# Kernel optimization log

Measured on AMD Instinct MI355X. Metric: run time of the kernel, lower is better.

## Reference

```python
import jax, jax.numpy as jnp
import numpy as np

N, E, G = 20000, 320000, 64
F_NODE, F_EDGE = 16, 16
NHID, M, NLAYER, NOUT = 128, 4, 3, 64
EPS = 1e-5


def setup_inputs() -> dict:
    key = jax.random.key(0)
    ks = jax.random.split(key, 20)
    w = lambda k, s: (jax.random.normal(k, s, jnp.float32) * 0.1)
    inp = {
        "x_node": jax.random.normal(ks[0], (N, F_NODE), jnp.float32),
        "edge_attr": jax.random.normal(ks[1], (E, F_EDGE), jnp.float32),
        "edge_index": jax.random.randint(ks[2], (2, E), 0, N, dtype=jnp.int32),
        "batch": jnp.sort(jax.random.randint(ks[3], (N,), 0, G, dtype=jnp.int32)),
        "additional_x": jax.random.normal(ks[4], (N, 1, M), jnp.float32),
        # input encoder MLP(F_NODE->NHID, 1 layer): Linear + BN + ReLU
        "W_in": w(ks[5], (NHID, F_NODE)), "b_in": jnp.zeros((NHID,)),
        "g_in": jnp.ones((NHID,)), "bt_in": jnp.zeros((NHID,)),
        # Linear2: weight (NHID, NHID+1), bias (NHID,)
        "W_l2": w(ks[6], (NHID, NHID + 1)), "b_l2": jnp.zeros((NHID,)),
        # per-layer edge encoders MLP(F_EDGE->NHID, 1 layer)
        "W_edge": w(ks[7], (NLAYER, NHID, F_EDGE)), "b_edge": jnp.zeros((NLAYER, NHID)),
        "g_edge": jnp.ones((NLAYER, NHID)), "bt_edge": jnp.zeros((NLAYER, NHID)),
        # per-layer conv linear (bias=False since bn='BN')
        "W_conv": w(ks[8], (NLAYER, NHID, NHID)),
        # per-layer BatchNorm1d(NHID)
        "g_norm": jnp.ones((NLAYER, NHID)), "bt_norm": jnp.zeros((NLAYER, NHID)),
        # output encoder MLP(NHID->NOUT, 2 layers, norm between, no final act)
        "W_out1": w(ks[9], (NOUT, NHID)), "b_out1": jnp.zeros((NOUT,)),
        "g_out": jnp.ones((NOUT,)), "bt_out": jnp.zeros((NOUT,)),
        "W_out2": w(ks[10], (NOUT, NOUT)), "b_out2": jnp.zeros((NOUT,)),
    }
    return inp


def _bn2(x, g, b):  # BatchNorm1d on (R, C), training-mode batch stats
    mu = x.mean(0)
    var = x.var(0)
    return (x - mu) * jax.lax.rsqrt(var + EPS) * g + b


def _bn3(x, g, b):  # BatchNorm1d on (N, C, M): stats over N and M per channel
    mu = x.mean((0, 2), keepdims=True)
    var = x.var((0, 2), keepdims=True)
    return (x - mu) * jax.lax.rsqrt(var + EPS) * g[None, :, None] + b[None, :, None]


def reference(x_node, edge_attr, edge_index, batch, additional_x,
              W_in, b_in, g_in, bt_in, W_l2, b_l2,
              W_edge, b_edge, g_edge, bt_edge, W_conv, g_norm, bt_norm,
              W_out1, b_out1, g_out, bt_out, W_out2, b_out2):
    # --- input encoder: MLP(F_node -> nhid, 1 layer) ---
    h = jax.nn.relu(_bn2(x_node @ W_in.T + b_in, g_in, bt_in))  # (N, NHID)

    # --- Linear2(h, additional_x): faithful to the torch reshapes ---
    n, d = h.shape
    m = additional_x.shape[-1]
    xr = jnp.transpose(additional_x, (2, 1, 0)).reshape(n * m, 1)  # x_r.T.reshape(N*M, -1)
    rand_out = xr @ W_l2[:, -1:].T + b_l2                          # (M*N, NHID)
    main = h @ W_l2[:, :-1] + b_l2                                 # F.linear(x, weight.T[:-1]) == x @ W[:, :-1]
    x = main[:, :, None] + rand_out.reshape(n, -1, m)              # (N, NHID, M)

    src, dst = edge_index[0], edge_index[1]
    prev = x
    for l in range(NLAYER):
        # edge encoder: MLP(F_edge -> nhid, 1 layer)
        e = jax.nn.relu(_bn2(edge_attr @ W_edge[l].T + b_edge[l], g_edge[l], bt_edge[l]))  # (E, NHID)
        # GINE-style conv: sum_j relu(x_j + e_ij), then linear on channel dim (no bias)
        msg = jax.nn.relu(x[src] + e[:, :, None])                  # (E, NHID, M)
        agg = jax.ops.segment_sum(msg, dst, num_segments=n)        # (N, NHID, M)
        h3 = jnp.einsum('ncm,oc->nom', x + agg, W_conv[l])
        h3 = jax.nn.relu(_bn3(h3, g_norm[l], bt_norm[l]))          # norm -> relu (dropout=0)
        x = h3 + prev                                              # residual
        prev = x

    # --- add pooling over graphs ---
    xg = jax.ops.segment_sum(x, batch, num_segments=G)             # (G, NHID, M)
    H1, H2, Mm = xg.shape
    flat = xg.reshape(-1, H2)                                      # faithful to x.view(-1, H2)
    o = jax.nn.relu(_bn2(flat @ W_out1.T + b_out1, g_out, bt_out))
    o = o @ W_out2.T + b_out2                                      # (G*M, NOUT)
    out = o.reshape(H1, o.shape[-1], -1).mean(-1)                  # (G, NOUT)
    return out
```

## Files before the change

kernel.cpp:

```cpp
#include <hip/hip_runtime.h>

constexpr int N_ = 20000, E_ = 320000, G_ = 64;
constexpr int NHID = 128, M_ = 4;
constexpr float EPS = 1e-5f;

#define RFL(v) __builtin_amdgcn_readfirstlane(v)
#define RLF(v, l) __int_as_float(__builtin_amdgcn_readlane(__float_as_int(v), (l)))

__global__ void k_moments(const float* __restrict__ A, int R,
                          float* __restrict__ oSum, float* __restrict__ oOut) {
  __shared__ float ls[64][16];
  int t = threadIdx.x;
  int k = t >> 4, j = t & 15;
  float accO = 0.f, accS = 0.f;
  for (int base = blockIdx.x * 64; base < R; base += gridDim.x * 64) {
    int rows = min(64, R - base);
    for (int i = t; i < rows * 16; i += 256) ls[i >> 4][i & 15] = A[base * 16 + i];
    __syncthreads();
    for (int r = 0; r < rows; ++r) accO += ls[r][k] * ls[r][j];
    if (t < 16) { for (int r = 0; r < rows; ++r) accS += ls[r][t]; }
    __syncthreads();
  }
  atomicAdd(&oOut[t], accO);
  if (t < 16) atomicAdd(&oSum[t], accS);
}

__global__ __launch_bounds__(512) void k_fold(
    const float* __restrict__ momNs, const float* __restrict__ momNo,
    const float* __restrict__ momEs, const float* __restrict__ momEo,
    const float* __restrict__ W_in, const float* __restrict__ b_in,
    const float* __restrict__ g_in, const float* __restrict__ bt_in,
    const float* __restrict__ W_e, const float* __restrict__ b_e,
    const float* __restrict__ g_e, const float* __restrict__ bt_e,
    float* __restrict__ Wf_in, float* __restrict__ bf_in,
    float* __restrict__ Wf_e, float* __restrict__ bf_e) {
  __shared__ float mN[16], oN[256], mE[16], oE[256];
  int t = threadIdx.x;
  if (t < 16) { mN[t] = momNs[t] * (1.f / N_); mE[t] = momEs[t] * (1.f / E_); }
  for (int i = t; i < 256; i += 512) { oN[i] = momNo[i] * (1.f / N_); oE[i] = momEo[i] * (1.f / E_); }
  __syncthreads();
  const float *m, *mo, *wrow; float bb, ggv, btv; float *wout, *boutp;
  if (t < 128) {
    m = mN; mo = oN; wrow = W_in + t * 16; bb = b_in[t]; ggv = g_in[t]; btv = bt_in[t];
    wout = Wf_in + t * 16; boutp = bf_in + t;
  } else {
    int u = t - 128;
    m = mE; mo = oE; wrow = W_e + u * 16; bb = b_e[u]; ggv = g_e[u]; btv = bt_e[u];
    wout = Wf_e + u * 16; boutp = bf_e + u;
  }
  float wl[16];
#pragma unroll
  for (int k = 0; k < 16; ++k) wl[k] = wrow[k];
  float wm = 0.f;
#pragma unroll
  for (int k = 0; k < 16; ++k) wm = fmaf(wl[k], m[k], wm);
  float mu = wm + bb;
  float ey2 = bb * bb + 2.f * bb * wm;
  for (int k = 0; k < 16; ++k) {
#pragma unroll
    for (int j = 0; j < 16; ++j) ey2 = fmaf(wl[k] * wl[j], mo[k * 16 + j], ey2);
  }
  float var = ey2 - mu * mu;
  float s = ggv * rsqrtf(var + EPS);
#pragma unroll
  for (int k = 0; k < 16; ++k) wout[k] = wl[k] * s;
  *boutp = (bb - mu) * s + btv;
}

__global__ __launch_bounds__(128) void k_lin2(
    const float* __restrict__ xn, const float* __restrict__ addx,
    const float* __restrict__ Wf, const float* __restrict__ bf,
    const float* __restrict__ W2, const float* __restrict__ b2,
    float* __restrict__ X) {
  __shared__ float a[4][16];
  __shared__ float h[4][128];
  int c = threadIdx.x;
  int n0 = blockIdx.x * 4;
  if (c < 64) a[c >> 4][c & 15] = xn[n0 * 16 + c];
  __syncthreads();
  float wl[16];
  const float* w = Wf + c * 16;
#pragma unroll
  for (int k = 0; k < 16; ++k) wl[k] = w[k];
  float bfc = bf[c];
#pragma unroll
  for (int nd = 0; nd < 4; ++nd) {
    float acc = bfc;
#pragma unroll
    for (int k = 0; k < 16; ++k) acc = fmaf(a[nd][k], wl[k], acc);
    h[nd][c] = fmaxf(acc, 0.f);
  }
  __syncthreads();
  float b2c = b2[c];
  float mn[4] = {b2c, b2c, b2c, b2c};
#pragma unroll 4
  for (int k = 0; k < 128; ++k) {
    float wv = W2[k * 129 + c];
    mn[0] = fmaf(h[0][k], wv, mn[0]);
    mn[1] = fmaf(h[1][k], wv, mn[1]);
    mn[2] = fmaf(h[2][k], wv, mn[2]);
    mn[3] = fmaf(h[3][k], wv, mn[3]);
  }
  int ccb = (c & 31) * 4;
  float wr0 = W2[(ccb + 0) * 129 + 128], br0 = b2[ccb + 0];
  float wr1 = W2[(ccb + 1) * 129 + 128], br1 = b2[ccb + 1];
  float wr2 = W2[(ccb + 2) * 129 + 128], br2 = b2[ccb + 2];
  float wr3 = W2[(ccb + 3) * 129 + 128], br3 = b2[ccb + 3];
  float4* Xv = reinterpret_cast<float4*>(X);
#pragma unroll
  for (int nd = 0; nd < 4; ++nd) {
    int i = 4 * (n0 + nd) + (c >> 5);
    int id = i / N_;
    int ir = i - id * N_;
    float xr = addx[ir * 4 + id];
    float4 o;
    o.x = mn[nd] + xr * wr0 + br0;
    o.y = mn[nd] + xr * wr1 + br1;
    o.z = mn[nd] + xr * wr2 + br2;
    o.w = mn[nd] + xr * wr3 + br3;
    Xv[(size_t)(n0 + nd) * 128 + c] = o;
  }
}

__global__ void k_hist(const int* __restrict__ ei, int* __restrict__ cnt) {
  int e = blockIdx.x * 256 + threadIdx.x;
  if (e < E_) atomicAdd(&cnt[ei[E_ + e]], 1);
}

__global__ __launch_bounds__(1024) void k_scan(const int* __restrict__ cnt, int* __restrict__ off) {
  __shared__ int wsum[16];
  __shared__ int carrySh;
  int t = threadIdx.x, lane = t & 63, w = t >> 6;
  if (t == 0) carrySh = 0;
  __syncthreads();
  for (int base = 0; base < N_; base += 1024) {
    int v = (base + t < N_) ? cnt[base + t] : 0;
    int s = v;
#pragma unroll
    for (int ofs = 1; ofs < 64; ofs <<= 1) {
      int u = __shfl_up(s, ofs);
      if (lane >= ofs) s += u;
    }
    if (lane == 63) wsum[w] = s;
    int carry = carrySh;
    __syncthreads();
    int pre = 0, tot = 0;
#pragma unroll
    for (int ww = 0; ww < 16; ++ww) {
      int x = wsum[ww];
      pre += (ww < w) ? x : 0;
      tot += x;
    }
    if (base + t < N_) off[base + t] = carry + pre + s - v;
    __syncthreads();
    if (t == 0) carrySh = carry + tot;
    __syncthreads();
  }
  if (t == 0) off[N_] = carrySh;
}

__global__ void k_scatter(const int* __restrict__ ei, const int* __restrict__ off,
                          int* __restrict__ cur, int* __restrict__ csr) {
  int e = blockIdx.x * 256 + threadIdx.x;
  if (e < E_) {
    int d = ei[E_ + e];
    int pidx = atomicAdd(&cur[d], 1);
    csr[off[d] + pidx] = e;
  }
}

__global__ void k_transp(const float* __restrict__ Wc, float* __restrict__ WT4) {
  int i = blockIdx.x * 256 + threadIdx.x;
  if (i >= 3 * 128 * 128) return;
  int l = i >> 14, rest = i & 16383;
  int o = rest >> 7, c = rest & 127;
  WT4[l * 16384 + ((c >> 1) * 64 + (o & 63)) * 4 + (c & 1) * 2 + (o >> 6)] = Wc[i];
}

__global__ void k_init64(int* g) { g[threadIdx.x] = N_; }
__global__ void k_bound(const int* __restrict__ batch, int* __restrict__ gstart) {
  int n = blockIdx.x * 256 + threadIdx.x;
  if (n < N_) atomicMin(&gstart[batch[n]], n);
}
__global__ void k_bound2(const int* __restrict__ gstart, int* __restrict__ gend) {
  int g = threadIdx.x;
  int e = N_;
  for (int gg = g + 1; gg < 64; ++gg) { int s = gstart[gg]; if (s < N_) { e = s; break; } }
  gend[g] = e;
}

__global__ __launch_bounds__(512, 4) void k_aggemm(
    const float* __restrict__ X, const int* __restrict__ ei,
    const float* __restrict__ attr,
    const int* __restrict__ off, const int* __restrict__ csr,
    const float* __restrict__ Wf, const float* __restrict__ bf,
    const float* __restrict__ WT4,
    float* __restrict__ H3, float* __restrict__ bnsum, float* __restrict__ bnsumsq) {
  __shared__ float lW[16384];
  __shared__ float red[512][4];
  int t = threadIdx.x;
  int lane = t & 63;
  int n = blockIdx.x * 8 + (t >> 6);
  {
    const float4* Wg = reinterpret_cast<const float4*>(WT4);
    float4* lW4 = reinterpret_cast<float4*>(lW);
#pragma unroll
    for (int i = 0; i < 8; ++i) lW4[t + i * 512] = Wg[t + i * 512];
  }
  float w0[16], w1[16];
#pragma unroll
  for (int k = 0; k < 16; ++k) { w0[k] = Wf[lane * 16 + k]; w1[k] = Wf[(lane + 64) * 16 + k]; }
  float b0 = bf[lane], b1 = bf[lane + 64];
  const float4* Xv = reinterpret_cast<const float4*>(X);
  const float4* Av = reinterpret_cast<const float4*>(attr);
  float4 acc0 = Xv[(size_t)n * 128 + lane];
  float4 acc1 = Xv[(size_t)n * 128 + 64 + lane];
  __syncthreads();

  int qs = RFL(off[n]);
  int qe = RFL(off[n + 1]);
  if (qs < qe) {
    int last = qe - 1;
#define IDX(Q, EV, SV) { int qq_ = (Q) < last ? (Q) : last; EV = RFL(csr[qq_]); SV = RFL(ei[EV]); }
#define LOADP(SV, EV, X0, X1, AV) \
    X0 = Xv[(size_t)(SV) * 128 + lane]; \
    X1 = Xv[(size_t)(SV) * 128 + 64 + lane]; \
    AV = Av[(size_t)(EV) * 4 + (lane & 3)];
#define ETERM(AVV, CMP, LN, K) { float as_ = RLF(AVV.CMP, LN); \
    ee0 = fmaf(as_, w0[K], ee0); ee1 = fmaf(as_, w1[K], ee1); }
#define EDGE(X0, X1, AV) { \
    float ee0 = b0, ee1 = b1; \
    ETERM(AV, x, 0, 0)  ETERM(AV, y, 0, 1)  ETERM(AV, z, 0, 2)  ETERM(AV, w, 0, 3) \
    ETERM(AV, x, 1, 4)  ETERM(AV, y, 1, 5)  ETERM(AV, z, 1, 6)  ETERM(AV, w, 1, 7) \
    ETERM(AV, x, 2, 8)  ETERM(AV, y, 2, 9)  ETERM(AV, z, 2, 10) ETERM(AV, w, 2, 11) \
    ETERM(AV, x, 3, 12) ETERM(AV, y, 3, 13) ETERM(AV, z, 3, 14) ETERM(AV, w, 3, 15) \
    ee0 = fmaxf(ee0, 0.f); ee1 = fmaxf(ee1, 0.f); \
    acc0.x += fmaxf(X0.x + ee0, 0.f); acc0.y += fmaxf(X0.y + ee0, 0.f); \
    acc0.z += fmaxf(X0.z + ee0, 0.f); acc0.w += fmaxf(X0.w + ee0, 0.f); \
    acc1.x += fmaxf(X1.x + ee1, 0.f); acc1.y += fmaxf(X1.y + ee1, 0.f); \
    acc1.z += fmaxf(X1.z + ee1, 0.f); acc1.w += fmaxf(X1.w + ee1, 0.f); }
    int e0, s0, e1, s1, e2, s2, e3, s3, e4, s4, e5, s5;
    IDX(qs,     e0, s0); IDX(qs + 1, e1, s1); IDX(qs + 2, e2, s2);
    IDX(qs + 3, e3, s3); IDX(qs + 4, e4, s4); IDX(qs + 5, e5, s5);
    float4 x00, x01, av0, x10, x11, av1, x20, x21, av2;
    LOADP(s0, e0, x00, x01, av0);
    LOADP(s1, e1, x10, x11, av1);
    LOADP(s2, e2, x20, x21, av2);
    for (int q = qs; q < qe; q += 3) {
      int n0i, n0s, n1i, n1s, n2i, n2s;
      IDX(q + 6, n0i, n0s); IDX(q + 7, n1i, n1s); IDX(q + 8, n2i, n2s);
      EDGE(x00, x01, av0);
      LOADP(s3, e3, x00, x01, av0);
      if (q + 1 < qe) { EDGE(x10, x11, av1); }
      LOADP(s4, e4, x10, x11, av1);
      if (q + 2 < qe) { EDGE(x20, x21, av2); }
      LOADP(s5, e5, x20, x21, av2);
      e0 = e3; s0 = s3; e1 = e4; s1 = s4; e2 = e5; s2 = s5;
      e3 = n0i; s3 = n0s; e4 = n1i; s4 = n1s; e5 = n2i; s5 = n2s;
    }
#undef EDGE
#undef ETERM
#undef LOADP
#undef IDX
  }
  float4 ha = {0, 0, 0, 0}, hb = {0, 0, 0, 0};
  const float4* Wv = reinterpret_cast<const float4*>(lW);
#pragma unroll 4
  for (int cc = 0; cc < 32; ++cc) {
    float4 wv = Wv[cc * 64 + lane];
    int l0 = 2 * cc, l1 = 2 * cc + 1;
    float za0 = RLF(acc0.x, l0), za1 = RLF(acc0.y, l0), za2 = RLF(acc0.z, l0), za3 = RLF(acc0.w, l0);
    float zb0 = RLF(acc0.x, l1), zb1 = RLF(acc0.y, l1), zb2 = RLF(acc0.z, l1), zb3 = RLF(acc0.w, l1);
    ha.x = fmaf(za0, wv.x, ha.x); ha.y = fmaf(za1, wv.x, ha.y); ha.z = fmaf(za2, wv.x, ha.z); ha.w = fmaf(za3, wv.x, ha.w);
    hb.x = fmaf(za0, wv.y, hb.x); hb.y = fmaf(za1, wv.y, hb.y); hb.z = fmaf(za2, wv.y, hb.z); hb.w = fmaf(za3, wv.y, hb.w);
    ha.x = fmaf(zb0, wv.z, ha.x); ha.y = fmaf(zb1, wv.z, ha.y); ha.z = fmaf(zb2, wv.z, ha.z); ha.w = fmaf(zb3, wv.z, ha.w);
    hb.x = fmaf(zb0, wv.w, hb.x); hb.y = fmaf(zb1, wv.w, hb.y); hb.z = fmaf(zb2, wv.w, hb.z); hb.w = fmaf(zb3, wv.w, hb.w);
  }
#pragma unroll 4
  for (int cc = 32; cc < 64; ++cc) {
    float4 wv = Wv[cc * 64 + lane];
    int l0 = 2 * cc - 64, l1 = 2 * cc - 63;
    float za0 = RLF(acc1.x, l0), za1 = RLF(acc1.y, l0), za2 = RLF(acc1.z, l0), za3 = RLF(acc1.w, l0);
    float zb0 = RLF(acc1.x, l1), zb1 = RLF(acc1.y, l1), zb2 = RLF(acc1.z, l1), zb3 = RLF(acc1.w, l1);
    ha.x = fmaf(za0, wv.x, ha.x); ha.y = fmaf(za1, wv.x, ha.y); ha.z = fmaf(za2, wv.x, ha.z); ha.w = fmaf(za3, wv.x, ha.w);
    hb.x = fmaf(za0, wv.y, hb.x); hb.y = fmaf(za1, wv.y, hb.y); hb.z = fmaf(za2, wv.y, hb.z); hb.w = fmaf(za3, wv.y, hb.w);
    ha.x = fmaf(zb0, wv.z, ha.x); ha.y = fmaf(zb1, wv.z, ha.y); ha.z = fmaf(zb2, wv.z, ha.z); ha.w = fmaf(zb3, wv.z, ha.w);
    hb.x = fmaf(zb0, wv.w, hb.x); hb.y = fmaf(zb1, wv.w, hb.y); hb.z = fmaf(zb2, wv.w, hb.z); hb.w = fmaf(zb3, wv.w, hb.w);
  }
  float4* Hv = reinterpret_cast<float4*>(H3);
  Hv[(size_t)n * 128 + lane] = ha;
  Hv[(size_t)n * 128 + 64 + lane] = hb;
  red[t][0] = ha.x + ha.y + ha.z + ha.w;
  red[t][1] = ha.x * ha.x + ha.y * ha.y + ha.z * ha.z + ha.w * ha.w;
  red[t][2] = hb.x + hb.y + hb.z + hb.w;
  red[t][3] = hb.x * hb.x + hb.y * hb.y + hb.z * hb.z + hb.w * hb.w;
  __syncthreads();
  if (t < 256) {
    int ch = t >> 1, st = t & 1;
    int ln = ch & 63, pr = ch >> 6;
    float v = 0.f;
#pragma unroll
    for (int w8 = 0; w8 < 8; ++w8) v += red[w8 * 64 + ln][pr * 2 + st];
    if (st == 0) atomicAdd(&bnsum[ch], v); else atomicAdd(&bnsumsq[ch], v);
  }
}

__global__ void k_bnres(const float* __restrict__ H3, float* __restrict__ X,
                        const float* __restrict__ bnsum, const float* __restrict__ bnsumsq,
                        const float* __restrict__ gg, const float* __restrict__ bb) {
  constexpr float inv = 1.f / (N_ * 4);
  const float4* Hv = (const float4*)H3;
  float4* Xv = (float4*)X;
  for (int i = blockIdx.x * 256 + threadIdx.x; i < N_ * 128; i += gridDim.x * 256) {
    int o = i & 127;
    float mu = bnsum[o] * inv;
    float var = bnsumsq[o] * inv - mu * mu;
    float sc = gg[o] * rsqrtf(var + EPS);
    float sh = bb[o] - mu * sc;
    float4 h = Hv[i];
    float4 x = Xv[i];
    x.x += fmaxf(fmaf(h.x, sc, sh), 0.f);
    x.y += fmaxf(fmaf(h.y, sc, sh), 0.f);
    x.z += fmaxf(fmaf(h.z, sc, sh), 0.f);
    x.w += fmaxf(fmaf(h.w, sc, sh), 0.f);
    Xv[i] = x;
  }
}

__global__ void k_pool(const float* __restrict__ X, const int* __restrict__ gstart,
                       const int* __restrict__ gend, float* __restrict__ xg) {
  int g = blockIdx.x >> 3, sl = blockIdx.x & 7;
  int t = threadIdx.x;
  int s = gstart[g], e = gend[g];
  float a0 = 0.f, a1 = 0.f;
  for (int n = s + sl; n < e; n += 8) {
    a0 += X[(size_t)n * 512 + t];
    a1 += X[(size_t)n * 512 + t + 256];
  }
  atomicAdd(&xg[g * 512 + t], a0);
  atomicAdd(&xg[g * 512 + t + 256], a1);
}

__global__ void k_head1(const float* __restrict__ xg, const float* __restrict__ W1,
                        const float* __restrict__ b1, float* __restrict__ o1p,
                        float* __restrict__ hsum, float* __restrict__ hsumsq) {
  int t = threadIdx.x;
  int r = blockIdx.x * 4 + (t >> 6), c = t & 63;
  const float* xr = xg + r * 128;
  const float* w = W1 + c * 128;
  float acc = b1[c];
#pragma unroll 8
  for (int k = 0; k < 128; ++k) acc = fmaf(xr[k], w[k], acc);
  o1p[r * 64 + c] = acc;
  atomicAdd(&hsum[c], acc);
  atomicAdd(&hsumsq[c], acc * acc);
}

__global__ void k_head2(const float* __restrict__ o1p, const float* __restrict__ hsum,
                        const float* __restrict__ hsumsq, const float* __restrict__ g_out,
                        const float* __restrict__ bt_out, const float* __restrict__ W2,
                        const float* __restrict__ b2, float* __restrict__ out) {
  __shared__ float s1[4][64];
  __shared__ float s2[4][64];
  int g = blockIdx.x, j = threadIdx.x;
  float mu = hsum[j] * (1.f / 256.f);
  float var = hsumsq[j] * (1.f / 256.f) - mu * mu;
  float sc = g_out[j] * rsqrtf(var + EPS);
  float sh = bt_out[j] - mu * sc;
  for (int r = 0; r < 4; ++r) {
    float v = o1p[(4 * g + r) * 64 + j];
    s1[r][j] = fmaxf(fmaf(v, sc, sh), 0.f);
  }
  __syncthreads();
  for (int r = 0; r < 4; ++r) {
    float acc = b2[j];
#pragma unroll 8
    for (int k = 0; k < 64; ++k) acc = fmaf(s1[r][k], W2[j * 64 + k], acc);
    s2[r][j] = acc;
  }
  __syncthreads();
  float o = 0.f;
#pragma unroll
  for (int k = 0; k < 4; ++k) {
    int t4 = 4 * j + k;
    o += s2[t4 >> 6][t4 & 63];
  }
  out[g * 64 + j] = o * 0.25f;
}

extern "C" void kernel_launch(void* const* d_in, const int* in_sizes, int n_in,
                              void* d_out, int out_size, void* d_ws, size_t ws_size,
                              hipStream_t stream) {
  const float* x_node   = (const float*)d_in[0];
  const float* edge_attr= (const float*)d_in[1];
  const int*   edge_index=(const int*)d_in[2];
  const int*   batch    = (const int*)d_in[3];
  const float* addx     = (const float*)d_in[4];
  const float* W_in  = (const float*)d_in[5];
  const float* b_in  = (const float*)d_in[6];
  const float* g_in  = (const float*)d_in[7];
  const float* bt_in = (const float*)d_in[8];
  const float* W_l2  = (const float*)d_in[9];
  const float* b_l2  = (const float*)d_in[10];
  const float* W_edge  = (const float*)d_in[11];
  const float* b_edge  = (const float*)d_in[12];
  const float* g_edge  = (const float*)d_in[13];
  const float* bt_edge = (const float*)d_in[14];
  const float* W_conv  = (const float*)d_in[15];
  const float* g_norm  = (const float*)d_in[16];
  const float* bt_norm = (const float*)d_in[17];
  const float* W_out1  = (const float*)d_in[18];
  const float* b_out1  = (const float*)d_in[19];
  const float* g_out   = (const float*)d_in[20];
  const float* bt_out  = (const float*)d_in[21];
  const float* W_out2  = (const float*)d_in[22];
  const float* b_out2  = (const float*)d_in[23];
  float* out = (float*)d_out;

  char* base = (char*)d_ws;
  size_t p = 0;
  auto take = [&](size_t bytes) -> char* {
    char* r = base + p;
    p = (p + bytes + 255) & ~(size_t)255;
    return r;
  };
  int*   csr_cnt  = (int*)take((size_t)N_ * 4);
  int*   csr_cur  = (int*)take((size_t)N_ * 4);
  float* momNs    = (float*)take(16 * 4);
  float* momNo    = (float*)take(256 * 4);
  float* momEs    = (float*)take(16 * 4);
  float* momEo    = (float*)take(256 * 4);
  float* bnsum    = (float*)take(3 * 128 * 4);
  float* bnsumsq  = (float*)take(3 * 128 * 4);
  float* xg       = (float*)take(64 * 512 * 4);
  float* hsum     = (float*)take(64 * 4);
  float* hsumsq   = (float*)take(64 * 4);
  size_t zeroEnd = p;
  int*   gstart   = (int*)take(64 * 4);
  int*   gend     = (int*)take(64 * 4);
  int*   csr_off  = (int*)take((size_t)(N_ + 1) * 4);
  int*   csr_edges= (int*)take((size_t)E_ * 4);
  float* Wf_in    = (float*)take(128 * 16 * 4);
  float* bf_in    = (float*)take(128 * 4);
  float* Wf_e     = (float*)take(3 * 128 * 16 * 4);
  float* bf_e     = (float*)take(3 * 128 * 4);
  float* WT4      = (float*)take(3 * 128 * 128 * 4);
  float* o1p      = (float*)take(256 * 64 * 4);
  float* A        = (float*)take((size_t)N_ * 512 * 4);
  float* B        = (float*)take((size_t)N_ * 512 * 4);

  hipMemsetAsync(d_ws, 0, zeroEnd, stream);
  k_init64<<<1, 64, 0, stream>>>(gstart);
  k_moments<<<320, 256, 0, stream>>>(x_node, N_, momNs, momNo);
  k_moments<<<2048, 256, 0, stream>>>(edge_attr, E_, momEs, momEo);
  k_fold<<<1, 512, 0, stream>>>(momNs, momNo, momEs, momEo,
                                W_in, b_in, g_in, bt_in,
                                W_edge, b_edge, g_edge, bt_edge,
                                Wf_in, bf_in, Wf_e, bf_e);
  k_lin2<<<N_ / 4, 128, 0, stream>>>(x_node, addx, Wf_in, bf_in, W_l2, b_l2, A);
  k_hist<<<1250, 256, 0, stream>>>(edge_index, csr_cnt);
  k_scan<<<1, 1024, 0, stream>>>(csr_cnt, csr_off);
  k_scatter<<<1250, 256, 0, stream>>>(edge_index, csr_off, csr_cur, csr_edges);
  k_transp<<<192, 256, 0, stream>>>(W_conv, WT4);
  k_bound<<<79, 256, 0, stream>>>(batch, gstart);
  k_bound2<<<1, 64, 0, stream>>>(gstart, gend);
  for (int l = 0; l < 3; ++l) {
    k_aggemm<<<N_ / 8, 512, 0, stream>>>(A, edge_index, edge_attr, csr_off, csr_edges,
                                         Wf_e + l * 128 * 16, bf_e + l * 128,
                                         WT4 + l * 16384, B,
                                         bnsum + l * 128, bnsumsq + l * 128);
    k_bnres<<<2048, 256, 0, stream>>>(B, A, bnsum + l * 128, bnsumsq + l * 128,
                                      g_norm + l * 128, bt_norm + l * 128);
  }
  k_pool<<<512, 256, 0, stream>>>(A, gstart, gend, xg);
  k_head1<<<64, 256, 0, stream>>>(xg, W_out1, b_out1, o1p, hsum, hsumsq);
  k_head2<<<64, 64, 0, stream>>>(o1p, hsum, hsumsq, g_out, bt_out, W_out2, b_out2, out);
  (void)in_sizes; (void)n_in; (void)out_size; (void)ws_size;
}
```

Measured before the change: 832.4 us.

## Merge prep kernels into fewer launches, enlarge aggemm blocks, hoist BN scale

Fuses the moment, histogram, weight-transpose and graph-boundary kernels into one block-partitioned prep kernel. The scan is merged with the BN fold, and the CSR scatter with the Linear2 kernel, so about eleven launches become three. The graph-boundary computation now uses the sorted batch directly instead of atomicMin plus a second pass. Separately, k_aggemm grows to 1024-thread blocks of 16 nodes so each staged copy of the weight tile in LDS serves more nodes, and k_bnres computes the per-channel BN scale and shift once per block into shared memory. The larger aggemm blocks may lower occupancy or raise register pressure.

```diff
diff --git a/kernel.cpp b/kernel.cpp
--- a/kernel.cpp
+++ b/kernel.cpp
@@ -7,13 +7,12 @@
 #define RFL(v) __builtin_amdgcn_readfirstlane(v)
 #define RLF(v, l) __int_as_float(__builtin_amdgcn_readlane(__float_as_int(v), (l)))
 
-__global__ void k_moments(const float* __restrict__ A, int R,
-                          float* __restrict__ oSum, float* __restrict__ oOut) {
-  __shared__ float ls[64][16];
-  int t = threadIdx.x;
+__device__ __forceinline__ void moments_body(
+    const float* __restrict__ A, int R, float* __restrict__ oSum, float* __restrict__ oOut,
+    int bid, int nb, int t, float ls[64][16]) {
   int k = t >> 4, j = t & 15;
   float accO = 0.f, accS = 0.f;
-  for (int base = blockIdx.x * 64; base < R; base += gridDim.x * 64) {
+  for (int base = bid * 64; base < R; base += nb * 64) {
     int rows = min(64, R - base);
     for (int i = t; i < rows * 16; i += 256) ls[i >> 4][i & 15] = A[base * 16 + i];
     __syncthreads();
@@ -25,7 +24,41 @@
   if (t < 16) atomicAdd(&oSum[t], accS);
 }
 
-__global__ __launch_bounds__(512) void k_fold(
+__global__ __launch_bounds__(256) void k_prep(
+    const float* __restrict__ xn, const float* __restrict__ attr,
+    const int* __restrict__ ei, const int* __restrict__ batch,
+    const float* __restrict__ Wc,
+    float* __restrict__ momNs, float* __restrict__ momNo,
+    float* __restrict__ momEs, float* __restrict__ momEo,
+    int* __restrict__ cnt, float* __restrict__ WT4, int* __restrict__ gs) {
+  __shared__ float ls[64][16];
+  int b = blockIdx.x, t = threadIdx.x;
+  if (b < 320) {
+    moments_body(xn, N_, momNs, momNo, b, 320, t, ls);
+  } else if (b < 2368) {
+    moments_body(attr, E_, momEs, momEo, b - 320, 2048, t, ls);
+  } else if (b < 3618) {
+    int e = (b - 2368) * 256 + t;
+    if (e < E_) atomicAdd(&cnt[ei[E_ + e]], 1);
+  } else if (b < 3810) {
+    int i = (b - 3618) * 256 + t;
+    if (i < 3 * 128 * 128) {
+      int l = i >> 14, rest = i & 16383;
+      int o = rest >> 7, c = rest & 127;
+      WT4[l * 16384 + ((c >> 1) * 64 + (o & 63)) * 4 + (c & 1) * 2 + (o >> 6)] = Wc[i];
+    }
+  } else {
+    int n = (b - 3810) * 256 + t;
+    if (n < N_) {
+      int bn = batch[n];
+      int bp = (n == 0) ? -1 : batch[n - 1];
+      for (int g = bp + 1; g <= bn; ++g) gs[g] = n;
+      if (n == N_ - 1) { for (int g = bn + 1; g <= 64; ++g) gs[g] = N_; }
+    }
+  }
+}
+
+__global__ __launch_bounds__(1024) void k_fold_scan(
     const float* __restrict__ momNs, const float* __restrict__ momNo,
     const float* __restrict__ momEs, const float* __restrict__ momEo,
     const float* __restrict__ W_in, const float* __restrict__ b_in,
@@ -33,50 +66,97 @@
     const float* __restrict__ W_e, const float* __restrict__ b_e,
     const float* __restrict__ g_e, const float* __restrict__ bt_e,
     float* __restrict__ Wf_in, float* __restrict__ bf_in,
-    float* __restrict__ Wf_e, float* __restrict__ bf_e) {
-  __shared__ float mN[16], oN[256], mE[16], oE[256];
+    float* __restrict__ Wf_e, float* __restrict__ bf_e,
+    const int* __restrict__ cnt, int* __restrict__ off) {
   int t = threadIdx.x;
-  if (t < 16) { mN[t] = momNs[t] * (1.f / N_); mE[t] = momEs[t] * (1.f / E_); }
-  for (int i = t; i < 256; i += 512) { oN[i] = momNo[i] * (1.f / N_); oE[i] = momEo[i] * (1.f / E_); }
-  __syncthreads();
-  const float *m, *mo, *wrow; float bb, ggv, btv; float *wout, *boutp;
-  if (t < 128) {
-    m = mN; mo = oN; wrow = W_in + t * 16; bb = b_in[t]; ggv = g_in[t]; btv = bt_in[t];
-    wout = Wf_in + t * 16; boutp = bf_in + t;
+  if (blockIdx.x == 0) {
+    __shared__ int wsum[16];
+    __shared__ int carrySh;
+    int lane = t & 63, w = t >> 6;
+    if (t == 0) carrySh = 0;
+    __syncthreads();
+    for (int base = 0; base < N_; base += 1024) {
+      int v = (base + t < N_) ? cnt[base + t] : 0;
+      int s = v;
+#pragma unroll
+      for (int ofs = 1; ofs < 64; ofs <<= 1) {
+        int u = __shfl_up(s, ofs);
+        if (lane >= ofs) s += u;
+      }
+      if (lane == 63) wsum[w] = s;
+      int carry = carrySh;
+      __syncthreads();
+      int pre = 0, tot = 0;
+#pragma unroll
+      for (int ww = 0; ww < 16; ++ww) {
+        int x = wsum[ww];
+        pre += (ww < w) ? x : 0;
+        tot += x;
+      }
+      if (base + t < N_) off[base + t] = carry + pre + s - v;
+      __syncthreads();
+      if (t == 0) carrySh = carry + tot;
+      __syncthreads();
+    }
+    if (t == 0) off[N_] = carrySh;
   } else {
-    int u = t - 128;
-    m = mE; mo = oE; wrow = W_e + u * 16; bb = b_e[u]; ggv = g_e[u]; btv = bt_e[u];
-    wout = Wf_e + u * 16; boutp = bf_e + u;
-  }
-  float wl[16];
-#pragma unroll
-  for (int k = 0; k < 16; ++k) wl[k] = wrow[k];
-  float wm = 0.f;
-#pragma unroll
-  for (int k = 0; k < 16; ++k) wm = fmaf(wl[k], m[k], wm);
-  float mu = wm + bb;
-  float ey2 = bb * bb + 2.f * bb * wm;
-  for (int k = 0; k < 16; ++k) {
-#pragma unroll
-    for (int j = 0; j < 16; ++j) ey2 = fmaf(wl[k] * wl[j], mo[k * 16 + j], ey2);
-  }
-  float var = ey2 - mu * mu;
-  float s = ggv * rsqrtf(var + EPS);
-#pragma unroll
-  for (int k = 0; k < 16; ++k) wout[k] = wl[k] * s;
-  *boutp = (bb - mu) * s + btv;
-}
-
-__global__ __launch_bounds__(128) void k_lin2(
+    __shared__ float mN[16], oN[256], mE[16], oE[256];
+    if (t < 16) { mN[t] = momNs[t] * (1.f / N_); mE[t] = momEs[t] * (1.f / E_); }
+    for (int i = t; i < 256; i += 1024) { oN[i] = momNo[i] * (1.f / N_); oE[i] = momEo[i] * (1.f / E_); }
+    __syncthreads();
+    if (t < 512) {
+      const float *m, *mo, *wrow; float bb, ggv, btv; float *wout, *boutp;
+      if (t < 128) {
+        m = mN; mo = oN; wrow = W_in + t * 16; bb = b_in[t]; ggv = g_in[t]; btv = bt_in[t];
+        wout = Wf_in + t * 16; boutp = bf_in + t;
+      } else {
+        int u = t - 128;
+        m = mE; mo = oE; wrow = W_e + u * 16; bb = b_e[u]; ggv = g_e[u]; btv = bt_e[u];
+        wout = Wf_e + u * 16; boutp = bf_e + u;
+      }
+      float wl[16];
+#pragma unroll
+      for (int k = 0; k < 16; ++k) wl[k] = wrow[k];
+      float wm = 0.f;
+#pragma unroll
+      for (int k = 0; k < 16; ++k) wm = fmaf(wl[k], m[k], wm);
+      float mu = wm + bb;
+      float ey2 = bb * bb + 2.f * bb * wm;
+      for (int k = 0; k < 16; ++k) {
+#pragma unroll
+        for (int j = 0; j < 16; ++j) ey2 = fmaf(wl[k] * wl[j], mo[k * 16 + j], ey2);
+      }
+      float var = ey2 - mu * mu;
+      float s = ggv * rsqrtf(var + EPS);
+#pragma unroll
+      for (int k = 0; k < 16; ++k) wout[k] = wl[k] * s;
+      *boutp = (bb - mu) * s + btv;
+    }
+  }
+}
+
+__global__ __launch_bounds__(256) void k_scat_lin2(
+    const int* __restrict__ ei, const int* __restrict__ off,
+    int* __restrict__ cur, int* __restrict__ csr,
     const float* __restrict__ xn, const float* __restrict__ addx,
     const float* __restrict__ Wf, const float* __restrict__ bf,
     const float* __restrict__ W2, const float* __restrict__ b2,
     float* __restrict__ X) {
-  __shared__ float a[4][16];
-  __shared__ float h[4][128];
-  int c = threadIdx.x;
-  int n0 = blockIdx.x * 4;
-  if (c < 64) a[c >> 4][c & 15] = xn[n0 * 16 + c];
+  int b = blockIdx.x, t = threadIdx.x;
+  if (b < 1250) {
+    int e = b * 256 + t;
+    if (e < E_) {
+      int d = ei[E_ + e];
+      int pidx = atomicAdd(&cur[d], 1);
+      csr[off[d] + pidx] = e;
+    }
+    return;
+  }
+  __shared__ float a[2][4][16];
+  __shared__ float h[2][4][128];
+  int sub = t >> 7, c = t & 127;
+  int n0 = (b - 1250) * 8 + sub * 4;
+  if (c < 64) a[sub][c >> 4][c & 15] = xn[(size_t)n0 * 16 + c];
   __syncthreads();
   float wl[16];
   const float* w = Wf + c * 16;
@@ -87,8 +167,8 @@
   for (int nd = 0; nd < 4; ++nd) {
     float acc = bfc;
 #pragma unroll
-    for (int k = 0; k < 16; ++k) acc = fmaf(a[nd][k], wl[k], acc);
-    h[nd][c] = fmaxf(acc, 0.f);
+    for (int k = 0; k < 16; ++k) acc = fmaf(a[sub][nd][k], wl[k], acc);
+    h[sub][nd][c] = fmaxf(acc, 0.f);
   }
   __syncthreads();
   float b2c = b2[c];
@@ -96,10 +176,10 @@
 #pragma unroll 4
   for (int k = 0; k < 128; ++k) {
     float wv = W2[k * 129 + c];
-    mn[0] = fmaf(h[0][k], wv, mn[0]);
-    mn[1] = fmaf(h[1][k], wv, mn[1]);
-    mn[2] = fmaf(h[2][k], wv, mn[2]);
-    mn[3] = fmaf(h[3][k], wv, mn[3]);
+    mn[0] = fmaf(h[sub][0][k], wv, mn[0]);
+    mn[1] = fmaf(h[sub][1][k], wv, mn[1]);
+    mn[2] = fmaf(h[sub][2][k], wv, mn[2]);
+    mn[3] = fmaf(h[sub][3][k], wv, mn[3]);
   }
   int ccb = (c & 31) * 4;
   float wr0 = W2[(ccb + 0) * 129 + 128], br0 = b2[ccb + 0];
@@ -122,74 +202,7 @@
   }
 }
 
-__global__ void k_hist(const int* __restrict__ ei, int* __restrict__ cnt) {
-  int e = blockIdx.x * 256 + threadIdx.x;
-  if (e < E_) atomicAdd(&cnt[ei[E_ + e]], 1);
-}
-
-__global__ __launch_bounds__(1024) void k_scan(const int* __restrict__ cnt, int* __restrict__ off) {
-  __shared__ int wsum[16];
-  __shared__ int carrySh;
-  int t = threadIdx.x, lane = t & 63, w = t >> 6;
-  if (t == 0) carrySh = 0;
-  __syncthreads();
-  for (int base = 0; base < N_; base += 1024) {
-    int v = (base + t < N_) ? cnt[base + t] : 0;
-    int s = v;
-#pragma unroll
-    for (int ofs = 1; ofs < 64; ofs <<= 1) {
-      int u = __shfl_up(s, ofs);
-      if (lane >= ofs) s += u;
-    }
-    if (lane == 63) wsum[w] = s;
-    int carry = carrySh;
-    __syncthreads();
-    int pre = 0, tot = 0;
-#pragma unroll
-    for (int ww = 0; ww < 16; ++ww) {
-      int x = wsum[ww];
-      pre += (ww < w) ? x : 0;
-      tot += x;
-    }
-    if (base + t < N_) off[base + t] = carry + pre + s - v;
-    __syncthreads();
-    if (t == 0) carrySh = carry + tot;
-    __syncthreads();
-  }
-  if (t == 0) off[N_] = carrySh;
-}
-
-__global__ void k_scatter(const int* __restrict__ ei, const int* __restrict__ off,
-                          int* __restrict__ cur, int* __restrict__ csr) {
-  int e = blockIdx.x * 256 + threadIdx.x;
-  if (e < E_) {
-    int d = ei[E_ + e];
-    int pidx = atomicAdd(&cur[d], 1);
-    csr[off[d] + pidx] = e;
-  }
-}
-
-__global__ void k_transp(const float* __restrict__ Wc, float* __restrict__ WT4) {
-  int i = blockIdx.x * 256 + threadIdx.x;
-  if (i >= 3 * 128 * 128) return;
-  int l = i >> 14, rest = i & 16383;
-  int o = rest >> 7, c = rest & 127;
-  WT4[l * 16384 + ((c >> 1) * 64 + (o & 63)) * 4 + (c & 1) * 2 + (o >> 6)] = Wc[i];
-}
-
-__global__ void k_init64(int* g) { g[threadIdx.x] = N_; }
-__global__ void k_bound(const int* __restrict__ batch, int* __restrict__ gstart) {
-  int n = blockIdx.x * 256 + threadIdx.x;
-  if (n < N_) atomicMin(&gstart[batch[n]], n);
-}
-__global__ void k_bound2(const int* __restrict__ gstart, int* __restrict__ gend) {
-  int g = threadIdx.x;
-  int e = N_;
-  for (int gg = g + 1; gg < 64; ++gg) { int s = gstart[gg]; if (s < N_) { e = s; break; } }
-  gend[g] = e;
-}
-
-__global__ __launch_bounds__(512, 4) void k_aggemm(
+__global__ __launch_bounds__(1024, 8) void k_aggemm(
     const float* __restrict__ X, const int* __restrict__ ei,
     const float* __restrict__ attr,
     const int* __restrict__ off, const int* __restrict__ csr,
@@ -197,15 +210,15 @@
     const float* __restrict__ WT4,
     float* __restrict__ H3, float* __restrict__ bnsum, float* __restrict__ bnsumsq) {
   __shared__ float lW[16384];
-  __shared__ float red[512][4];
+  __shared__ float red[1024][4];
   int t = threadIdx.x;
   int lane = t & 63;
-  int n = blockIdx.x * 8 + (t >> 6);
+  int n = blockIdx.x * 16 + (t >> 6);
   {
     const float4* Wg = reinterpret_cast<const float4*>(WT4);
     float4* lW4 = reinterpret_cast<float4*>(lW);
 #pragma unroll
-    for (int i = 0; i < 8; ++i) lW4[t + i * 512] = Wg[t + i * 512];
+    for (int i = 0; i < 4; ++i) lW4[t + i * 1024] = Wg[t + i * 1024];
   }
   float w0[16], w1[16];
 #pragma unroll
@@ -300,23 +313,31 @@
     int ln = ch & 63, pr = ch >> 6;
     float v = 0.f;
 #pragma unroll
-    for (int w8 = 0; w8 < 8; ++w8) v += red[w8 * 64 + ln][pr * 2 + st];
+    for (int w16 = 0; w16 < 16; ++w16) v += red[w16 * 64 + ln][pr * 2 + st];
     if (st == 0) atomicAdd(&bnsum[ch], v); else atomicAdd(&bnsumsq[ch], v);
   }
 }
 
-__global__ void k_bnres(const float* __restrict__ H3, float* __restrict__ X,
-                        const float* __restrict__ bnsum, const float* __restrict__ bnsumsq,
-                        const float* __restrict__ gg, const float* __restrict__ bb) {
+__global__ __launch_bounds__(256) void k_bnres(
+    const float* __restrict__ H3, float* __restrict__ X,
+    const float* __restrict__ bnsum, const float* __restrict__ bnsumsq,
+    const float* __restrict__ gg, const float* __restrict__ bb) {
   constexpr float inv = 1.f / (N_ * 4);
+  __shared__ float lsc[128], lsh[128];
+  int t = threadIdx.x;
+  if (t < 128) {
+    float mu = bnsum[t] * inv;
+    float var = bnsumsq[t] * inv - mu * mu;
+    float sc = gg[t] * rsqrtf(var + EPS);
+    lsc[t] = sc;
+    lsh[t] = bb[t] - mu * sc;
+  }
+  __syncthreads();
   const float4* Hv = (const float4*)H3;
   float4* Xv = (float4*)X;
-  for (int i = blockIdx.x * 256 + threadIdx.x; i < N_ * 128; i += gridDim.x * 256) {
+  for (int i = blockIdx.x * 256 + t; i < N_ * 128; i += gridDim.x * 256) {
     int o = i & 127;
-    float mu = bnsum[o] * inv;
-    float var = bnsumsq[o] * inv - mu * mu;
-    float sc = gg[o] * rsqrtf(var + EPS);
-    float sh = bb[o] - mu * sc;
+    float sc = lsc[o], sh = lsh[o];
     float4 h = Hv[i];
     float4 x = Xv[i];
     x.x += fmaxf(fmaf(h.x, sc, sh), 0.f);
@@ -327,11 +348,11 @@
   }
 }
 
-__global__ void k_pool(const float* __restrict__ X, const int* __restrict__ gstart,
-                       const int* __restrict__ gend, float* __restrict__ xg) {
+__global__ void k_pool(const float* __restrict__ X, const int* __restrict__ gs,
+                       float* __restrict__ xg) {
   int g = blockIdx.x >> 3, sl = blockIdx.x & 7;
   int t = threadIdx.x;
-  int s = gstart[g], e = gend[g];
+  int s = gs[g], e = gs[g + 1];
   float a0 = 0.f, a1 = 0.f;
   for (int n = s + sl; n < e; n += 8) {
     a0 += X[(size_t)n * 512 + t];
@@ -436,8 +457,7 @@
   float* hsum     = (float*)take(64 * 4);
   float* hsumsq   = (float*)take(64 * 4);
   size_t zeroEnd = p;
-  int*   gstart   = (int*)take(64 * 4);
-  int*   gend     = (int*)take(64 * 4);
+  int*   gs       = (int*)take(65 * 4);
   int*   csr_off  = (int*)take((size_t)(N_ + 1) * 4);
   int*   csr_edges= (int*)take((size_t)E_ * 4);
   float* Wf_in    = (float*)take(128 * 16 * 4);
@@ -450,29 +470,24 @@
   float* B        = (float*)take((size_t)N_ * 512 * 4);
 
   hipMemsetAsync(d_ws, 0, zeroEnd, stream);
-  k_init64<<<1, 64, 0, stream>>>(gstart);
-  k_moments<<<320, 256, 0, stream>>>(x_node, N_, momNs, momNo);
-  k_moments<<<2048, 256, 0, stream>>>(edge_attr, E_, momEs, momEo);
-  k_fold<<<1, 512, 0, stream>>>(momNs, momNo, momEs, momEo,
-                                W_in, b_in, g_in, bt_in,
-                                W_edge, b_edge, g_edge, bt_edge,
-                                Wf_in, bf_in, Wf_e, bf_e);
-  k_lin2<<<N_ / 4, 128, 0, stream>>>(x_node, addx, Wf_in, bf_in, W_l2, b_l2, A);
-  k_hist<<<1250, 256, 0, stream>>>(edge_index, csr_cnt);
-  k_scan<<<1, 1024, 0, stream>>>(csr_cnt, csr_off);
-  k_scatter<<<1250, 256, 0, stream>>>(edge_index, csr_off, csr_cur, csr_edges);
-  k_transp<<<192, 256, 0, stream>>>(W_conv, WT4);
-  k_bound<<<79, 256, 0, stream>>>(batch, gstart);
-  k_bound2<<<1, 64, 0, stream>>>(gstart, gend);
+  k_prep<<<3889, 256, 0, stream>>>(x_node, edge_attr, edge_index, batch, W_conv,
+                                   momNs, momNo, momEs, momEo, csr_cnt, WT4, gs);
+  k_fold_scan<<<2, 1024, 0, stream>>>(momNs, momNo, momEs, momEo,
+                                      W_in, b_in, g_in, bt_in,
+                                      W_edge, b_edge, g_edge, bt_edge,
+                                      Wf_in, bf_in, Wf_e, bf_e,
+                                      csr_cnt, csr_off);
+  k_scat_lin2<<<3750, 256, 0, stream>>>(edge_index, csr_off, csr_cur, csr_edges,
+                                        x_node, addx, Wf_in, bf_in, W_l2, b_l2, A);
   for (int l = 0; l < 3; ++l) {
-    k_aggemm<<<N_ / 8, 512, 0, stream>>>(A, edge_index, edge_attr, csr_off, csr_edges,
-                                         Wf_e + l * 128 * 16, bf_e + l * 128,
-                                         WT4 + l * 16384, B,
-                                         bnsum + l * 128, bnsumsq + l * 128);
+    k_aggemm<<<N_ / 16, 1024, 0, stream>>>(A, edge_index, edge_attr, csr_off, csr_edges,
+                                           Wf_e + l * 128 * 16, bf_e + l * 128,
+                                           WT4 + l * 16384, B,
+                                           bnsum + l * 128, bnsumsq + l * 128);
     k_bnres<<<2048, 256, 0, stream>>>(B, A, bnsum + l * 128, bnsumsq + l * 128,
                                       g_norm + l * 128, bt_norm + l * 128);
   }
-  k_pool<<<512, 256, 0, stream>>>(A, gstart, gend, xg);
+  k_pool<<<512, 256, 0, stream>>>(A, gs, xg);
   k_head1<<<64, 256, 0, stream>>>(xg, W_out1, b_out1, o1p, hsum, hsumsq);
   k_head2<<<64, 64, 0, stream>>>(o1p, hsum, hsumsq, g_out, bt_out, W_out2, b_out2, out);
   (void)in_sizes; (void)n_in; (void)out_size; (void)ws_size;
```

Result: slower. 1.564 ms (+87.9%).
